# Performance work log

Measured on AMD Instinct MI355X. Metric: run time of the kernel, lower is better.

Reference implementation:

```python
import jax, jax.numpy as jnp
import numpy as np

N_IN = 512
N_OUT = 256
T = 2048
B = 32


def setup_inputs() -> dict:
    key = jax.random.key(0)
    ks = jax.random.split(key, 9)
    s_in = 1.0 / np.sqrt(N_IN)
    inp = {
        "xt": jax.random.normal(ks[0], (T, B, N_IN), dtype=jnp.float32),
        "ct_forward": jax.random.normal(ks[1], (1, B, N_OUT), dtype=jnp.float32),
        # weights stored torch-style as [out, in]
        "Wx": jax.random.uniform(ks[2], (N_OUT, N_IN), jnp.float32, -s_in, s_in),
        "Wf": jax.random.uniform(ks[3], (N_OUT, N_IN), jnp.float32, -s_in, s_in),
        "bf": jax.random.uniform(ks[4], (N_OUT,), jnp.float32, -s_in, s_in),
        "Wr": jax.random.uniform(ks[5], (N_OUT, N_IN), jnp.float32, -s_in, s_in),
        "br": jax.random.uniform(ks[6], (N_OUT,), jnp.float32, -s_in, s_in),
        "Wc": jax.random.uniform(ks[7], (N_OUT, N_IN), jnp.float32, -s_in, s_in),
        "bc": jax.random.uniform(ks[8], (N_OUT,), jnp.float32, -s_in, s_in),
    }
    return inp


def reference(xt, ct_forward, Wx, Wf, bf, Wr, br, Wc, bc):
    # Batched projections over all timesteps (the GEMM part of SRU).
    x_proj = jnp.einsum("tbi,oi->tbo", xt, Wx)              # [T,B,n_out]
    f = jax.nn.sigmoid(jnp.einsum("tbi,oi->tbo", xt, Wf) + bf)
    r = jax.nn.sigmoid(jnp.einsum("tbi,oi->tbo", xt, Wr) + br)
    cx = jnp.einsum("tbi,oi->tbo", xt, Wc) + bc

    def step(c, inp):
        x_t, ft, rt, cxt = inp
        c = ft * c + (1.0 - ft) * x_t
        h = rt * jnp.tanh(c) + (1.0 - rt) * cxt
        return c, h

    c_final, ht = jax.lax.scan(step, ct_forward[0], (x_proj, f, r, cx))
    # dropout=0.0 -> identity; forward returns (ht, ct)
    return ht, c_final
```

## Files before the change

kernel.cpp:

```cpp
#include <hip/hip_runtime.h>
#include <stdint.h>

#define T_STEPS 2048
#define BATCH   32
#define NIN     512
#define NOUT    256
#define MROWS   (T_STEPS*BATCH)
#define BO      (BATCH*NOUT)
#define NCHUNK  32
#define CHLEN   (T_STEPS/NCHUNK)

typedef _Float16 f16x8 __attribute__((ext_vector_type(8)));
typedef _Float16 f16x4 __attribute__((ext_vector_type(4)));
typedef float    fx4   __attribute__((ext_vector_type(4)));

#define LDSP(p) ((__attribute__((address_space(3))) void*)(p))
#define GLBP(p) ((const __attribute__((address_space(1))) void*)(p))

#define BAR()       asm volatile("s_barrier" ::: "memory")
#define WAITLGKM0() do { asm volatile("s_waitcnt lgkmcnt(0)" ::: "memory"); __builtin_amdgcn_sched_barrier(0); } while(0)
#define WAITVM(n)   do { asm volatile("s_waitcnt vmcnt(" #n ")" ::: "memory"); __builtin_amdgcn_sched_barrier(0); } while(0)

__global__ __launch_bounds__(256) void convert_x(
    const float* __restrict__ xt, _Float16* __restrict__ xh)
{
    long i = ((long)blockIdx.x * 256 + threadIdx.x) * 8;
    float4 v0 = *(const float4*)(xt + i);
    float4 v1 = *(const float4*)(xt + i + 4);
    f16x8 h;
    h[0] = (_Float16)v0.x; h[1] = (_Float16)v0.y;
    h[2] = (_Float16)v0.z; h[3] = (_Float16)v0.w;
    h[4] = (_Float16)v1.x; h[5] = (_Float16)v1.y;
    h[6] = (_Float16)v1.z; h[7] = (_Float16)v1.w;
    *(f16x8*)(xh + i) = h;
}

__global__ __launch_bounds__(256) void convert_w(
    const float* __restrict__ Wx, const float* __restrict__ Wf,
    const float* __restrict__ Wr, const float* __restrict__ Wc,
    _Float16* __restrict__ Wcat)
{
    int idx = blockIdx.x * 256 + threadIdx.x;
    int n  = idx >> 7;
    int k4 = (idx & 127) * 4;
    int g = n >> 8, o = n & 255;
    const float* W = (g == 0) ? Wx : (g == 1) ? Wf : (g == 2) ? Wr : Wc;
    float4 v = *(const float4*)(W + o * NIN + k4);
    f16x4 h;
    h[0] = (_Float16)v.x; h[1] = (_Float16)v.y;
    h[2] = (_Float16)v.z; h[3] = (_Float16)v.w;
    *(f16x4*)(Wcat + n * NIN + k4) = h;
}

#define BM 256
#define BN 256
#define BK 64
#define NGT 32

__global__ __launch_bounds__(512) void gemm_proj(
    const _Float16* __restrict__ xh,
    const _Float16* __restrict__ Wcat,
    const float* __restrict__ bfv, const float* __restrict__ brv, const float* __restrict__ bcv,
    _Float16* __restrict__ xp_h, _Float16* __restrict__ f_h,
    _Float16* __restrict__ r_h,  _Float16* __restrict__ cx_h)
{
    __shared__ char lds[131072];

    const int tid  = threadIdx.x;
    const int lane = tid & 63;
    const int w    = tid >> 6;
    const int wrq  = w >> 2;
    const int wcq  = w & 3;
    const int lr = lane & 15, lk = lane >> 4;

    int wg = (blockIdx.x & 7) * 32 + (blockIdx.x >> 3);
    const int  cg   = wg & 3;
    const int  mgrp = wg >> 2;
    const long m0 = (long)mgrp * 1024;
    const int  n0 = cg * BN;

    const int rl8  = lane >> 3;
    const int scol = (((lane & 7) ^ rl8) << 4);
    const char* baseA = (const char*)xh   + (m0 + w * 8 + rl8) * 1024 + scol;
    const char* baseB = (const char*)Wcat + ((long)(n0 + w * 8 + rl8)) * 1024 + scol;

#define STAGE_A(g, h) do {                                                   \
        char* _d = lds + ((g) & 1) * 32768 + (h) * 16384 + w * 1024;         \
        const char* _s = baseA + (long)((g) >> 3) * 262144                   \
                         + ((g) & 7) * 128 + (long)(h) * 131072;             \
        __builtin_amdgcn_global_load_lds(GLBP(_s),         LDSP(_d),        16, 0, 0); \
        __builtin_amdgcn_global_load_lds(GLBP(_s + 65536), LDSP(_d + 8192), 16, 0, 0); \
    } while (0)
#define STAGE_B(g, h) do {                                                   \
        char* _d = lds + 65536 + ((g) & 1) * 32768 + (h) * 16384 + w * 1024; \
        const char* _s = baseB + ((g) & 7) * 128 + (long)(h) * 131072;       \
        __builtin_amdgcn_global_load_lds(GLBP(_s),         LDSP(_d),        16, 0, 0); \
        __builtin_amdgcn_global_load_lds(GLBP(_s + 65536), LDSP(_d + 8192), 16, 0, 0); \
    } while (0)

    fx4 acc[2][2][4][2];
    #pragma unroll
    for (int a = 0; a < 2; ++a)
        #pragma unroll
        for (int b = 0; b < 2; ++b)
            #pragma unroll
            for (int c = 0; c < 4; ++c)
                #pragma unroll
                for (int d = 0; d < 2; ++d)
                    acc[a][b][c][d] = (fx4){0.f, 0.f, 0.f, 0.f};

    f16x8 Ar[4][2];
    f16x8 B0r[2][2];
    f16x8 B1r[2][2];

#define READ_A(c2, h) do {                                                   \
        _Pragma("unroll")                                                    \
        for (int mf = 0; mf < 4; ++mf) {                                     \
            int rl = wrq * 64 + mf * 16 + lr;                                \
            int rb = (c2) * 32768 + (h) * 16384 + rl * 128;                  \
            _Pragma("unroll")                                                \
            for (int kk = 0; kk < 2; ++kk)                                   \
                Ar[mf][kk] = *(const f16x8*)(lds + rb +                      \
                    ((kk * 64 + lk * 16) ^ ((rl & 7) << 4)));                \
        }                                                                    \
    } while (0)
#define READ_B(c2, h, dst) do {                                              \
        _Pragma("unroll")                                                    \
        for (int nf = 0; nf < 2; ++nf) {                                     \
            int rl = wcq * 32 + nf * 16 + lr;                                \
            int rb = 65536 + (c2) * 32768 + (h) * 16384 + rl * 128;          \
            _Pragma("unroll")                                                \
            for (int kk = 0; kk < 2; ++kk)                                   \
                dst[nf][kk] = *(const f16x8*)(lds + rb +                     \
                    ((kk * 64 + lk * 16) ^ ((rl & 7) << 4)));                \
        }                                                                    \
    } while (0)
#define MMACC(Qr, Qc, Br) do {                                               \
        __builtin_amdgcn_s_setprio(1);                                       \
        _Pragma("unroll")                                                    \
        for (int kk = 0; kk < 2; ++kk)                                       \
            _Pragma("unroll")                                                \
            for (int mf = 0; mf < 4; ++mf)                                   \
                _Pragma("unroll")                                            \
                for (int nf = 0; nf < 2; ++nf)                               \
                    acc[Qr][Qc][mf][nf] = __builtin_amdgcn_mfma_f32_16x16x32_f16( \
                        Br[nf][kk], Ar[mf][kk], acc[Qr][Qc][mf][nf], 0, 0, 0);    \
        __builtin_amdgcn_s_setprio(0);                                       \
    } while (0)

    const int g_out = cg;
    _Float16* outp = (g_out == 0) ? xp_h : (g_out == 1) ? f_h : (g_out == 2) ? r_h : cx_h;
    const float* bias = (g_out == 1) ? bfv : (g_out == 2) ? brv : (g_out == 3) ? bcv : nullptr;

    STAGE_A(0, 0); STAGE_B(0, 0); STAGE_B(0, 1); STAGE_A(0, 1);
    STAGE_A(1, 0); STAGE_B(1, 0);
    WAITVM(4);
    BAR();

    for (int g = 0; g < NGT; ++g) {
        const int c2 = g & 1;
        READ_A(c2, 0);
        READ_B(c2, 0, B0r);
        if (g + 1 < NGT) STAGE_B(g + 1, 1);
        WAITLGKM0();
        MMACC(0, 0, B0r);
        READ_B(c2, 1, B1r);
        if (g + 1 < NGT) STAGE_A(g + 1, 1);
        WAITLGKM0();
        MMACC(0, 1, B1r);
        READ_A(c2, 1);
        BAR();
        if (g + 2 < NGT) STAGE_A(g + 2, 0);
        WAITLGKM0();
        MMACC(1, 0, B0r);
        if (g + 2 < NGT) STAGE_B(g + 2, 0);
        MMACC(1, 1, B1r);
        if (g < NGT - 2)       WAITVM(4);
        else if (g == NGT - 2) WAITVM(0);
        BAR();
        if ((g & 7) == 7) {
            const long mbase = m0 + (long)(g >> 3) * 256;
            #pragma unroll
            for (int Qr = 0; Qr < 2; ++Qr) {
                #pragma unroll
                for (int Qc = 0; Qc < 2; ++Qc) {
                    #pragma unroll
                    for (int nf = 0; nf < 2; ++nf) {
                        const int ob = Qc * 128 + wcq * 32 + nf * 16 + lk * 4;
                        float4 bv4 = (g_out == 0) ? (float4){0.f, 0.f, 0.f, 0.f}
                                                  : *(const float4*)(bias + ob);
                        #pragma unroll
                        for (int mf = 0; mf < 4; ++mf) {
                            long row = mbase + Qr * 128 + wrq * 64 + mf * 16 + lr;
                            fx4 v = acc[Qr][Qc][mf][nf];
                            f16x4 hv;
                            if (g_out == 1 || g_out == 2) {
                                float p0 = v[0] + bv4.x, p1 = v[1] + bv4.y;
                                float p2 = v[2] + bv4.z, p3 = v[3] + bv4.w;
                                hv[0] = (_Float16)(__builtin_amdgcn_rcpf(1.0f + __expf(-p0)));
                                hv[1] = (_Float16)(__builtin_amdgcn_rcpf(1.0f + __expf(-p1)));
                                hv[2] = (_Float16)(__builtin_amdgcn_rcpf(1.0f + __expf(-p2)));
                                hv[3] = (_Float16)(__builtin_amdgcn_rcpf(1.0f + __expf(-p3)));
                            } else {
                                hv[0] = (_Float16)(v[0] + bv4.x);
                                hv[1] = (_Float16)(v[1] + bv4.y);
                                hv[2] = (_Float16)(v[2] + bv4.z);
                                hv[3] = (_Float16)(v[3] + bv4.w);
                            }
                            *(f16x4*)(outp + row * NOUT + ob) = hv;
                            acc[Qr][Qc][mf][nf] = (fx4){0.f, 0.f, 0.f, 0.f};
                        }
                    }
                }
            }
        }
    }
}

__global__ __launch_bounds__(256) void chunk_scan_a(
    const _Float16* __restrict__ f_h, const _Float16* __restrict__ xp_h,
    float* __restrict__ chunkA, float* __restrict__ chunkB)
{
    int tid = blockIdx.x * 256 + threadIdx.x;
    int chunk = tid >> 13;
    int bo = tid & (BO - 1);
    long base = (long)chunk * CHLEN * BO + bo;
    float a = 1.f, cc = 0.f;
    #pragma unroll 4
    for (int s = 0; s < CHLEN; ++s) {
        long i = base + (long)s * BO;
        float fv = (float)f_h[i];
        float xv = (float)xp_h[i];
        cc = fv * cc + (1.f - fv) * xv;
        a *= fv;
    }
    chunkA[tid] = a;
    chunkB[tid] = cc;
}

__global__ __launch_bounds__(256) void chunk_prop(
    const float* __restrict__ ct0,
    const float* __restrict__ chunkA, const float* __restrict__ chunkB,
    float* __restrict__ cin, float* __restrict__ c_final)
{
    int bo = blockIdx.x * 256 + threadIdx.x;
    float c = ct0[bo];
    #pragma unroll
    for (int ch = 0; ch < NCHUNK; ++ch) {
        cin[ch * BO + bo] = c;
        c = chunkA[ch * BO + bo] * c + chunkB[ch * BO + bo];
    }
    c_final[bo] = c;
}

__global__ __launch_bounds__(256) void chunk_scan_h(
    const _Float16* __restrict__ xp_h, const _Float16* __restrict__ f_h,
    const _Float16* __restrict__ r_h,  const _Float16* __restrict__ cx_h,
    const float* __restrict__ cin, float* __restrict__ ht)
{
    int tid = blockIdx.x * 256 + threadIdx.x;
    int chunk = tid >> 13;
    int bo = tid & (BO - 1);
    long base = (long)chunk * CHLEN * BO + bo;
    float c = cin[tid];
    #pragma unroll 4
    for (int s = 0; s < CHLEN; ++s) {
        long i = base + (long)s * BO;
        float fv = (float)f_h[i];
        float xv = (float)xp_h[i];
        float rv = (float)r_h[i];
        float cxv = (float)cx_h[i];
        c = fv * c + (1.f - fv) * xv;
        float e = __expf(2.f * c);
        float th = (e - 1.f) * __builtin_amdgcn_rcpf(e + 1.f);
        ht[i] = rv * th + (1.f - rv) * cxv;
    }
}

extern "C" void kernel_launch(void* const* d_in, const int* in_sizes, int n_in,
                              void* d_out, int out_size, void* d_ws, size_t ws_size,
                              hipStream_t stream) {
    const float* xt  = (const float*)d_in[0];
    const float* ct0 = (const float*)d_in[1];
    const float* Wx  = (const float*)d_in[2];
    const float* Wf  = (const float*)d_in[3];
    const float* bf_ = (const float*)d_in[4];
    const float* Wr  = (const float*)d_in[5];
    const float* br_ = (const float*)d_in[6];
    const float* Wc  = (const float*)d_in[7];
    const float* bc_ = (const float*)d_in[8];

    float* ht      = (float*)d_out;
    float* c_final = ht + (size_t)MROWS * NOUT;

    char* ws = (char*)d_ws;
    _Float16* Wcat = (_Float16*)ws;
    _Float16* xh   = (_Float16*)(ws + (1 << 20));
    _Float16* xp_h = xh + (size_t)MROWS * NIN;
    _Float16* f_h  = xp_h + (size_t)MROWS * NOUT;
    _Float16* r_h  = f_h  + (size_t)MROWS * NOUT;
    _Float16* cx_h = r_h  + (size_t)MROWS * NOUT;
    float* chunkA  = (float*)(cx_h + (size_t)MROWS * NOUT);
    float* chunkB  = chunkA + NCHUNK * BO;
    float* cin     = chunkB + NCHUNK * BO;

    convert_w<<<512, 256, 0, stream>>>(Wx, Wf, Wr, Wc, Wcat);
    convert_x<<<(MROWS * NIN / 8) / 256, 256, 0, stream>>>(xt, xh);
    gemm_proj<<<256, 512, 0, stream>>>(
        xh, Wcat, bf_, br_, bc_, xp_h, f_h, r_h, cx_h);
    chunk_scan_a<<<(NCHUNK * BO) / 256, 256, 0, stream>>>(f_h, xp_h, chunkA, chunkB);
    chunk_prop<<<BO / 256, 256, 0, stream>>>(ct0, chunkA, chunkB, cin, c_final);
    chunk_scan_h<<<(NCHUNK * BO) / 256, 256, 0, stream>>>(xp_h, f_h, r_h, cx_h, cin, ht);
}
```

Measured before the change: 188.9 us.

## Restructure GEMM main loop to issue all stages early and batch MFMAs

```diff
diff --git a/kernel.cpp b/kernel.cpp
--- a/kernel.cpp
+++ b/kernel.cpp
@@ -17,9 +17,9 @@
 #define LDSP(p) ((__attribute__((address_space(3))) void*)(p))
 #define GLBP(p) ((const __attribute__((address_space(1))) void*)(p))
 
-#define BAR()       asm volatile("s_barrier" ::: "memory")
-#define WAITLGKM0() do { asm volatile("s_waitcnt lgkmcnt(0)" ::: "memory"); __builtin_amdgcn_sched_barrier(0); } while(0)
-#define WAITVM(n)   do { asm volatile("s_waitcnt vmcnt(" #n ")" ::: "memory"); __builtin_amdgcn_sched_barrier(0); } while(0)
+#define BAR()        asm volatile("s_barrier" ::: "memory")
+#define DRAIN_LGKM() asm volatile("s_waitcnt lgkmcnt(0)" ::: "memory")
+#define WAITVM(n)    do { asm volatile("s_waitcnt vmcnt(" #n ")" ::: "memory"); __builtin_amdgcn_sched_barrier(0); } while(0)
 
 __global__ __launch_bounds__(256) void convert_x(
     const float* __restrict__ xt, _Float16* __restrict__ xh)
@@ -57,7 +57,7 @@
 #define BK 64
 #define NGT 32
 
-__global__ __launch_bounds__(512) void gemm_proj(
+__global__ __launch_bounds__(512, 2) void gemm_proj(
     const _Float16* __restrict__ xh,
     const _Float16* __restrict__ Wcat,
     const float* __restrict__ bfv, const float* __restrict__ brv, const float* __restrict__ bcv,
@@ -109,18 +109,19 @@
                 for (int d = 0; d < 2; ++d)
                     acc[a][b][c][d] = (fx4){0.f, 0.f, 0.f, 0.f};
 
-    f16x8 Ar[4][2];
+    f16x8 Ar0[4][2];
+    f16x8 Ar1[4][2];
     f16x8 B0r[2][2];
     f16x8 B1r[2][2];
 
-#define READ_A(c2, h) do {                                                   \
+#define READ_A(c2, h, dst) do {                                              \
         _Pragma("unroll")                                                    \
         for (int mf = 0; mf < 4; ++mf) {                                     \
             int rl = wrq * 64 + mf * 16 + lr;                                \
             int rb = (c2) * 32768 + (h) * 16384 + rl * 128;                  \
             _Pragma("unroll")                                                \
             for (int kk = 0; kk < 2; ++kk)                                   \
-                Ar[mf][kk] = *(const f16x8*)(lds + rb +                      \
+                dst[mf][kk] = *(const f16x8*)(lds + rb +                     \
                     ((kk * 64 + lk * 16) ^ ((rl & 7) << 4)));                \
         }                                                                    \
     } while (0)
@@ -135,8 +136,7 @@
                     ((kk * 64 + lk * 16) ^ ((rl & 7) << 4)));                \
         }                                                                    \
     } while (0)
-#define MMACC(Qr, Qc, Br) do {                                               \
-        __builtin_amdgcn_s_setprio(1);                                       \
+#define MMACC(Qr, Qc, Aa, Br) do {                                           \
         _Pragma("unroll")                                                    \
         for (int kk = 0; kk < 2; ++kk)                                       \
             _Pragma("unroll")                                                \
@@ -144,8 +144,7 @@
                 _Pragma("unroll")                                            \
                 for (int nf = 0; nf < 2; ++nf)                               \
                     acc[Qr][Qc][mf][nf] = __builtin_amdgcn_mfma_f32_16x16x32_f16( \
-                        Br[nf][kk], Ar[mf][kk], acc[Qr][Qc][mf][nf], 0, 0, 0);    \
-        __builtin_amdgcn_s_setprio(0);                                       \
+                        Br[nf][kk], Aa[mf][kk], acc[Qr][Qc][mf][nf], 0, 0, 0);    \
     } while (0)
 
     const int g_out = cg;
@@ -159,22 +158,18 @@
 
     for (int g = 0; g < NGT; ++g) {
         const int c2 = g & 1;
-        READ_A(c2, 0);
+        READ_A(c2, 0, Ar0);
         READ_B(c2, 0, B0r);
-        if (g + 1 < NGT) STAGE_B(g + 1, 1);
-        WAITLGKM0();
-        MMACC(0, 0, B0r);
+        DRAIN_LGKM();
+        BAR();
+        if (g + 1 < NGT) { STAGE_B(g + 1, 1); STAGE_A(g + 1, 1); }
+        if (g + 2 < NGT) { STAGE_A(g + 2, 0); STAGE_B(g + 2, 0); }
         READ_B(c2, 1, B1r);
-        if (g + 1 < NGT) STAGE_A(g + 1, 1);
-        WAITLGKM0();
-        MMACC(0, 1, B1r);
-        READ_A(c2, 1);
-        BAR();
-        if (g + 2 < NGT) STAGE_A(g + 2, 0);
-        WAITLGKM0();
-        MMACC(1, 0, B0r);
-        if (g + 2 < NGT) STAGE_B(g + 2, 0);
-        MMACC(1, 1, B1r);
+        READ_A(c2, 1, Ar1);
+        MMACC(0, 0, Ar0, B0r);
+        MMACC(0, 1, Ar0, B1r);
+        MMACC(1, 0, Ar1, B0r);
+        MMACC(1, 1, Ar1, B1r);
         if (g < NGT - 2)       WAITVM(4);
         else if (g == NGT - 2) WAITVM(0);
         BAR();
```

Result: no change. 192.1 us (+1.7%).
